# Optimization experiments

Hardware: AMD Instinct MI355X
Metric: run time of the kernel (lower is better)

Reference implementation:

```python
import math
import jax, jax.numpy as jnp
import numpy as np
from jax.scipy.special import ndtri

D = 128          # head_dim
BITS = 4         # bits per coordinate
NLEV = 1 << BITS # 16 codebook levels


def pack_indices(idx, bits):
    # idx: (..., d) uint8 with values < 2**bits; bits=4 -> 2 indices per byte.
    per_byte = 8 // bits
    i = idx.reshape(*idx.shape[:-1], idx.shape[-1] // per_byte, per_byte).astype(jnp.uint8)
    shifts = (jnp.arange(per_byte, dtype=jnp.uint8) * bits)  # low nibble first
    packed = jnp.zeros(i.shape[:-1], dtype=jnp.uint8)
    for j in range(per_byte):
        packed = packed | (i[..., j] << shifts[j])
    return packed


def unpack_indices(packed, bits, d):
    per_byte = 8 // bits
    mask = jnp.uint8((1 << bits) - 1)
    parts = [((packed >> jnp.uint8(j * bits)) & mask) for j in range(per_byte)]
    idx = jnp.stack(parts, axis=-1)  # (..., d_packed, per_byte)
    return idx.reshape(*packed.shape[:-1], d)


def setup_inputs() -> dict:
    key = jax.random.key(0)
    kx, kp = jax.random.split(key)
    x = jax.random.normal(kx, (4, 8, 4096, D), dtype=jnp.float32)
    # Random rotation matrix via QR of a Gaussian (orthogonal, like get_rotation_matrix).
    A = jax.random.normal(kp, (D, D), dtype=jnp.float32)
    Pi, _ = jnp.linalg.qr(A)
    # Lloyd-Max-style Gaussian codebook: sorted inverse-CDF midpoints of N(0,1).
    codebook = ndtri((jnp.arange(NLEV, dtype=jnp.float32) + 0.5) / NLEV).astype(jnp.float32)
    return {"x": x, "Pi": Pi.astype(jnp.float32), "codebook": codebook}


def reference(x, Pi, codebook):
    d = x.shape[-1]
    sqrt_d = math.sqrt(d)
    # ---- compress ----
    norms = jnp.linalg.norm(x, axis=-1)                       # (*batch,)
    x_unit = x / jnp.clip(norms, 1e-8)[..., None]
    x_rot_scaled = (x_unit @ Pi.T) * sqrt_d                   # (*batch, d)
    dists = jnp.abs(x_rot_scaled[..., None] - codebook)      # (*batch, d, n_levels)
    indices = jnp.argmin(dists, axis=-1).astype(jnp.uint8)   # (*batch, d)
    packed = pack_indices(indices, BITS)                      # (*batch, d_packed) uint8
    norms16 = norms.astype(jnp.float16)
    # ---- decompress ----
    idx = unpack_indices(packed, BITS, d).astype(jnp.int32)
    x_rot_hat = codebook[idx] / sqrt_d                        # (*batch, d)
    x_unit_hat = x_rot_hat @ Pi
    x_hat = x_unit_hat * norms16.astype(jnp.float32)[..., None]
    return x_hat
```

## Files before the change

### kernel.cpp

```cpp
#include <hip/hip_runtime.h>
#include <hip/hip_fp16.h>
#include <cstdint>

#define D 128
#define NLEV 16
#define TPB 512
#define WPB 8
#define RPW 8
#define NBATCH 2
#define ROWS_PER_WAVE 16
#define ROWS_PER_BLOCK (WPB * ROWS_PER_WAVE)

typedef __attribute__((ext_vector_type(8))) short bf16x8;
typedef __attribute__((ext_vector_type(4))) float f32x4;

__device__ __forceinline__ float rlane_f(float v, int l) {
    return __int_as_float(__builtin_amdgcn_readlane(__float_as_int(v), l));
}
__device__ __forceinline__ float sload_f(float v) {
    return __int_as_float(__builtin_amdgcn_readfirstlane(__float_as_int(v)));
}
__device__ __forceinline__ unsigned short f32_bf16(float f) {
    uint32_t u = __float_as_uint(f);
    return (unsigned short)((u + 0x7fffu + ((u >> 16) & 1u)) >> 16);
}
__device__ __forceinline__ float bf16_f32(unsigned short h) {
    return __uint_as_float(((uint32_t)h) << 16);
}

__global__ void tq_prepack(const float* __restrict__ Pi, float* __restrict__ PiT,
                           unsigned short* __restrict__ Bhi, unsigned short* __restrict__ Blo) {
    const int t = blockIdx.x * blockDim.x + threadIdx.x;
    PiT[t] = Pi[(t & (D - 1)) * D + (t >> 7)];
    const int e = t & 7, l = (t >> 3) & 63, f = t >> 9;
    const int kf = f & 3, it = f >> 2;
    const int k = kf * 32 + (l >> 4) * 8 + e;
    const int i = it * 16 + (l & 15);
    const float v = Pi[k * D + i];
    const unsigned short hi = f32_bf16(v);
    Bhi[t] = hi;
    Blo[t] = f32_bf16(v - bf16_f32(hi));
}

__global__ __launch_bounds__(TPB, 3)
void tq_main(const float* __restrict__ x, const float* __restrict__ PiT,
             const unsigned short* __restrict__ Bhi, const unsigned short* __restrict__ Blo,
             const float* __restrict__ cbk, float* __restrict__ out, int nrows) {
    __shared__ uint32_t lds_u[8192];
    float* ldsP = (float*)lds_u;

    const int tid  = threadIdx.x;
    const int lane = tid & 63;
    const int wave = tid >> 6;

    float code[NLEV], mid[NLEV - 1];
#pragma unroll
    for (int k = 0; k < NLEV; ++k) code[k] = sload_f(cbk[k]);
#pragma unroll
    for (int k = 0; k < NLEV - 1; ++k) mid[k] = 0.5f * (code[k] + code[k + 1]);

    const float sqrt_d = 11.313708498984761f;

    const int row0 = (blockIdx.x * WPB + wave) * ROWS_PER_WAVE;

    float2 xv[NBATCH][RPW];
#pragma unroll
    for (int b = 0; b < NBATCH; ++b)
#pragma unroll
        for (int r = 0; r < RPW; ++r) {
            int row = row0 + b * RPW + r;
            if (row >= nrows) row = nrows - 1;
            xv[b][r] = *reinterpret_cast<const float2*>(x + (size_t)row * D + 2 * lane);
        }

    float ns[NBATCH][RPW];
#pragma unroll
    for (int b = 0; b < NBATCH; ++b)
#pragma unroll
        for (int r = 0; r < RPW; ++r) {
            float s = fmaf(xv[b][r].x, xv[b][r].x, xv[b][r].y * xv[b][r].y);
#pragma unroll
            for (int off = 32; off; off >>= 1) s += __shfl_xor(s, off, 64);
            ns[b][r] = s;
        }

    float y0[NBATCH][RPW], y1[NBATCH][RPW];
#pragma unroll
    for (int b = 0; b < NBATCH; ++b)
#pragma unroll
        for (int r = 0; r < RPW; ++r) { y0[b][r] = 0.f; y1[b][r] = 0.f; }

    for (int h = 0; h < 2; ++h) {
        __syncthreads();
        for (int kk = tid; kk < 64 * D; kk += TPB) ldsP[kk] = PiT[h * 64 * D + kk];
        __syncthreads();
#pragma unroll 4
        for (int jj = 0; jj < 64; jj += 2) {
            const float2 p0 = *reinterpret_cast<const float2*>(ldsP + jj * D + 2 * lane);
            const float2 p1 = *reinterpret_cast<const float2*>(ldsP + (jj + 1) * D + 2 * lane);
            const int sl = (h * 64 + jj) >> 1;
#pragma unroll
            for (int b = 0; b < NBATCH; ++b)
#pragma unroll
                for (int r = 0; r < RPW; ++r) {
                    const float xa = rlane_f(xv[b][r].x, sl);
                    const float xb = rlane_f(xv[b][r].y, sl);
                    y0[b][r] = fmaf(p0.x, xa, y0[b][r]);
                    y1[b][r] = fmaf(p0.y, xa, y1[b][r]);
                    y0[b][r] = fmaf(p1.x, xb, y0[b][r]);
                    y1[b][r] = fmaf(p1.y, xb, y1[b][r]);
                }
        }
    }

    uint32_t cpk[NBATCH][RPW];
#pragma unroll
    for (int b = 0; b < NBATCH; ++b)
#pragma unroll
        for (int r = 0; r < RPW; ++r) {
            const float nrm = sqrtf(ns[b][r]);
            const float s1  = sqrt_d / fmaxf(nrm, 1e-8f);
            const float hh  = __half2float(__float2half(nrm));
            const float sc  = hh / sqrt_d;
            const float ya = y0[b][r] * s1;
            const float yb = y1[b][r] * s1;
            float ca = code[0], cb2 = code[0];
#pragma unroll
            for (int k = 0; k < NLEV - 1; ++k) {
                ca  = (ya > mid[k]) ? code[k + 1] : ca;
                cb2 = (yb > mid[k]) ? code[k + 1] : cb2;
            }
            const unsigned short ha = __half_as_ushort(__float2half(ca * sc));
            const unsigned short hb = __half_as_ushort(__float2half(cb2 * sc));
            cpk[b][r] = (uint32_t)ha | ((uint32_t)hb << 16);
        }

    __syncthreads();

#pragma unroll
    for (int b = 0; b < NBATCH; ++b)
#pragma unroll
        for (int r = 0; r < RPW; ++r) {
            const int r16 = b * RPW + r;
            lds_u[(wave * 16 + r16) * 64 + (lane ^ ((r16 & 7) << 2))] = cpk[b][r];
        }
    __syncthreads();

    const int m  = lane & 15;
    const int kb = lane >> 4;
    bf16x8 ahi[4], alo[4];
#pragma unroll
    for (int kf = 0; kf < 4; ++kf) {
        const int idx = (wave * 16 + m) * 64 + ((kf * 16 + kb * 4) ^ ((m & 7) << 2));
        const uint4 u = *reinterpret_cast<const uint4*>(lds_u + idx);
#pragma unroll
        for (int q = 0; q < 4; ++q) {
            const uint32_t w = ((const uint32_t*)&u)[q];
            const float f0 = __half2float(__ushort_as_half((unsigned short)(w & 0xffffu)));
            const float f1 = __half2float(__ushort_as_half((unsigned short)(w >> 16)));
            const unsigned short h0 = f32_bf16(f0);
            const unsigned short h1 = f32_bf16(f1);
            ahi[kf][2 * q]     = (short)h0;
            ahi[kf][2 * q + 1] = (short)h1;
            alo[kf][2 * q]     = (short)f32_bf16(f0 - bf16_f32(h0));
            alo[kf][2 * q + 1] = (short)f32_bf16(f1 - bf16_f32(h1));
        }
    }
#pragma unroll
    for (int it = 0; it < 8; ++it) {
        f32x4 a = {0.f, 0.f, 0.f, 0.f};
#pragma unroll
        for (int kf = 0; kf < 4; ++kf) {
            const size_t fi = (size_t)((it * 4 + kf) * 64 + lane) * 8;
            const bf16x8 bh = *reinterpret_cast<const bf16x8*>(Bhi + fi);
            const bf16x8 bl = *reinterpret_cast<const bf16x8*>(Blo + fi);
            a = __builtin_amdgcn_mfma_f32_16x16x32_bf16(ahi[kf], bh, a, 0, 0, 0);
            a = __builtin_amdgcn_mfma_f32_16x16x32_bf16(alo[kf], bh, a, 0, 0, 0);
            a = __builtin_amdgcn_mfma_f32_16x16x32_bf16(ahi[kf], bl, a, 0, 0, 0);
        }
#pragma unroll
        for (int reg = 0; reg < 4; ++reg) {
            const int row = row0 + kb * 4 + reg;
            if (row < nrows) out[(size_t)row * D + it * 16 + m] = a[reg];
        }
    }
}

extern "C" void kernel_launch(void* const* d_in, const int* in_sizes, int n_in,
                              void* d_out, int out_size, void* d_ws, size_t ws_size,
                              hipStream_t stream) {
    const float* x   = (const float*)d_in[0];
    const float* Pi  = (const float*)d_in[1];
    const float* cbk = (const float*)d_in[2];
    float* out = (float*)d_out;

    float*          PiT = (float*)d_ws;
    unsigned short* Bhi = (unsigned short*)((char*)d_ws + 65536);
    unsigned short* Blo = (unsigned short*)((char*)d_ws + 98304);

    const int nrows = in_sizes[0] / D;
    const int grid  = (nrows + ROWS_PER_BLOCK - 1) / ROWS_PER_BLOCK;

    tq_prepack<<<dim3(64), dim3(256), 0, stream>>>(Pi, PiT, Bhi, Blo);
    tq_main<<<dim3(grid), dim3(TPB), 0, stream>>>(x, PiT, Bhi, Blo, cbk, out, nrows);
}
```

Baseline: 234.7 us.

## Replace readlane broadcasts with uniform global loads and pair-packed Pi layout

The rotation GEMV no longer broadcasts x elements with per-row readlane. Each wave instead reads the x values it needs as wave-uniform float2 loads from global memory (cached). Pi is repacked so one float4 LDS load supplies two columns by two k-values, which halves the LDS load count. Rows are clamped to full 16-row tiles, and launch bounds drop from 3 to 2 blocks per CU, allowing more registers at the cost of occupancy.

```diff
diff --git a/kernel.cpp b/kernel.cpp
--- a/kernel.cpp
+++ b/kernel.cpp
@@ -6,17 +6,12 @@
 #define NLEV 16
 #define TPB 512
 #define WPB 8
-#define RPW 8
-#define NBATCH 2
 #define ROWS_PER_WAVE 16
 #define ROWS_PER_BLOCK (WPB * ROWS_PER_WAVE)
 
 typedef __attribute__((ext_vector_type(8))) short bf16x8;
 typedef __attribute__((ext_vector_type(4))) float f32x4;
 
-__device__ __forceinline__ float rlane_f(float v, int l) {
-    return __int_as_float(__builtin_amdgcn_readlane(__float_as_int(v), l));
-}
 __device__ __forceinline__ float sload_f(float v) {
     return __int_as_float(__builtin_amdgcn_readfirstlane(__float_as_int(v)));
 }
@@ -28,10 +23,13 @@
     return __uint_as_float(((uint32_t)h) << 16);
 }
 
-__global__ void tq_prepack(const float* __restrict__ Pi, float* __restrict__ PiT,
+__global__ void tq_prepack(const float* __restrict__ Pi, float* __restrict__ PiTpair,
                            unsigned short* __restrict__ Bhi, unsigned short* __restrict__ Blo) {
     const int t = blockIdx.x * blockDim.x + threadIdx.x;
-    PiT[t] = Pi[(t & (D - 1)) * D + (t >> 7)];
+    {
+        const int q = t & 3, l = (t >> 2) & 63, jp = t >> 8;
+        PiTpair[t] = Pi[(2 * l + (q & 1)) * D + (2 * jp + (q >> 1))];
+    }
     const int e = t & 7, l = (t >> 3) & 63, f = t >> 9;
     const int kf = f & 3, it = f >> 2;
     const int k = kf * 32 + (l >> 4) * 8 + e;
@@ -42,8 +40,8 @@
     Blo[t] = f32_bf16(v - bf16_f32(hi));
 }
 
-__global__ __launch_bounds__(TPB, 3)
-void tq_main(const float* __restrict__ x, const float* __restrict__ PiT,
+__global__ __launch_bounds__(TPB, 2)
+void tq_main(const float* __restrict__ x, const float* __restrict__ PiTpair,
              const unsigned short* __restrict__ Bhi, const unsigned short* __restrict__ Blo,
              const float* __restrict__ cbk, float* __restrict__ out, int nrows) {
     __shared__ uint32_t lds_u[8192];
@@ -61,89 +59,80 @@
 
     const float sqrt_d = 11.313708498984761f;
 
-    const int row0 = (blockIdx.x * WPB + wave) * ROWS_PER_WAVE;
+    int row0 = (blockIdx.x * WPB + wave) * ROWS_PER_WAVE;
+    if (row0 > nrows - ROWS_PER_WAVE) row0 = nrows - ROWS_PER_WAVE;
 
-    float2 xv[NBATCH][RPW];
+    float ns[ROWS_PER_WAVE];
+    {
+        float2 xv[ROWS_PER_WAVE];
 #pragma unroll
-    for (int b = 0; b < NBATCH; ++b)
+        for (int r = 0; r < ROWS_PER_WAVE; ++r)
+            xv[r] = *reinterpret_cast<const float2*>(x + (size_t)(row0 + r) * D + 2 * lane);
 #pragma unroll
-        for (int r = 0; r < RPW; ++r) {
-            int row = row0 + b * RPW + r;
-            if (row >= nrows) row = nrows - 1;
-            xv[b][r] = *reinterpret_cast<const float2*>(x + (size_t)row * D + 2 * lane);
-        }
-
-    float ns[NBATCH][RPW];
-#pragma unroll
-    for (int b = 0; b < NBATCH; ++b)
-#pragma unroll
-        for (int r = 0; r < RPW; ++r) {
-            float s = fmaf(xv[b][r].x, xv[b][r].x, xv[b][r].y * xv[b][r].y);
+        for (int r = 0; r < ROWS_PER_WAVE; ++r) {
+            float s = fmaf(xv[r].x, xv[r].x, xv[r].y * xv[r].y);
 #pragma unroll
             for (int off = 32; off; off >>= 1) s += __shfl_xor(s, off, 64);
-            ns[b][r] = s;
+            ns[r] = s;
         }
+    }
 
-    float y0[NBATCH][RPW], y1[NBATCH][RPW];
+    float y0[ROWS_PER_WAVE], y1[ROWS_PER_WAVE];
 #pragma unroll
-    for (int b = 0; b < NBATCH; ++b)
-#pragma unroll
-        for (int r = 0; r < RPW; ++r) { y0[b][r] = 0.f; y1[b][r] = 0.f; }
+    for (int r = 0; r < ROWS_PER_WAVE; ++r) { y0[r] = 0.f; y1[r] = 0.f; }
+
+    const float* xw = x + (size_t)row0 * D;
 
     for (int h = 0; h < 2; ++h) {
         __syncthreads();
-        for (int kk = tid; kk < 64 * D; kk += TPB) ldsP[kk] = PiT[h * 64 * D + kk];
+        {
+            const float4* src = reinterpret_cast<const float4*>(PiTpair + h * 8192);
+            float4* dst = reinterpret_cast<float4*>(ldsP);
+#pragma unroll
+            for (int k = 0; k < 4; ++k) dst[tid + k * TPB] = src[tid + k * TPB];
+        }
         __syncthreads();
-#pragma unroll 4
-        for (int jj = 0; jj < 64; jj += 2) {
-            const float2 p0 = *reinterpret_cast<const float2*>(ldsP + jj * D + 2 * lane);
-            const float2 p1 = *reinterpret_cast<const float2*>(ldsP + (jj + 1) * D + 2 * lane);
-            const int sl = (h * 64 + jj) >> 1;
+#pragma unroll 2
+        for (int jp = 0; jp < 32; ++jp) {
+            const float4 p = reinterpret_cast<const float4*>(ldsP)[jp * 64 + lane];
+            const int j = h * 64 + jp * 2;
 #pragma unroll
-            for (int b = 0; b < NBATCH; ++b)
-#pragma unroll
-                for (int r = 0; r < RPW; ++r) {
-                    const float xa = rlane_f(xv[b][r].x, sl);
-                    const float xb = rlane_f(xv[b][r].y, sl);
-                    y0[b][r] = fmaf(p0.x, xa, y0[b][r]);
-                    y1[b][r] = fmaf(p0.y, xa, y1[b][r]);
-                    y0[b][r] = fmaf(p1.x, xb, y0[b][r]);
-                    y1[b][r] = fmaf(p1.y, xb, y1[b][r]);
-                }
+            for (int r = 0; r < ROWS_PER_WAVE; ++r) {
+                const float2 xj = *reinterpret_cast<const float2*>(xw + r * D + j);
+                y0[r] = fmaf(p.x, xj.x, y0[r]);
+                y1[r] = fmaf(p.y, xj.x, y1[r]);
+                y0[r] = fmaf(p.z, xj.y, y0[r]);
+                y1[r] = fmaf(p.w, xj.y, y1[r]);
+            }
         }
     }
 
-    uint32_t cpk[NBATCH][RPW];
+    uint32_t cpk[ROWS_PER_WAVE];
 #pragma unroll
-    for (int b = 0; b < NBATCH; ++b)
+    for (int r = 0; r < ROWS_PER_WAVE; ++r) {
+        const float nrm = sqrtf(ns[r]);
+        const float s1  = sqrt_d / fmaxf(nrm, 1e-8f);
+        const float hh  = __half2float(__float2half(nrm));
+        const float sc  = hh / sqrt_d;
+        const float ya = y0[r] * s1;
+        const float yb = y1[r] * s1;
+        float ca = code[0], cb2 = code[0];
 #pragma unroll
-        for (int r = 0; r < RPW; ++r) {
-            const float nrm = sqrtf(ns[b][r]);
-            const float s1  = sqrt_d / fmaxf(nrm, 1e-8f);
-            const float hh  = __half2float(__float2half(nrm));
-            const float sc  = hh / sqrt_d;
-            const float ya = y0[b][r] * s1;
-            const float yb = y1[b][r] * s1;
-            float ca = code[0], cb2 = code[0];
-#pragma unroll
-            for (int k = 0; k < NLEV - 1; ++k) {
-                ca  = (ya > mid[k]) ? code[k + 1] : ca;
-                cb2 = (yb > mid[k]) ? code[k + 1] : cb2;
-            }
-            const unsigned short ha = __half_as_ushort(__float2half(ca * sc));
-            const unsigned short hb = __half_as_ushort(__float2half(cb2 * sc));
-            cpk[b][r] = (uint32_t)ha | ((uint32_t)hb << 16);
+        for (int k = 0; k < NLEV - 1; ++k) {
+            ca  = (ya > mid[k]) ? code[k + 1] : ca;
+            cb2 = (yb > mid[k]) ? code[k + 1] : cb2;
         }
+        const unsigned short ha = __half_as_ushort(__float2half(ca * sc));
+        const unsigned short hb = __half_as_ushort(__float2half(cb2 * sc));
+        cpk[r] = (uint32_t)ha | ((uint32_t)hb << 16);
+    }
 
     __syncthreads();
 
 #pragma unroll
-    for (int b = 0; b < NBATCH; ++b)
-#pragma unroll
-        for (int r = 0; r < RPW; ++r) {
-            const int r16 = b * RPW + r;
-            lds_u[(wave * 16 + r16) * 64 + (lane ^ ((r16 & 7) << 2))] = cpk[b][r];
-        }
+    for (int r = 0; r < ROWS_PER_WAVE; ++r) {
+        lds_u[(wave * 16 + r) * 64 + (lane ^ ((r & 7) << 2))] = cpk[r];
+    }
     __syncthreads();
 
     const int m  = lane & 15;
@@ -194,13 +183,13 @@
     const float* cbk = (const float*)d_in[2];
     float* out = (float*)d_out;
 
-    float*          PiT = (float*)d_ws;
+    float*          PiTpair = (float*)d_ws;
     unsigned short* Bhi = (unsigned short*)((char*)d_ws + 65536);
     unsigned short* Blo = (unsigned short*)((char*)d_ws + 98304);
 
     const int nrows = in_sizes[0] / D;
     const int grid  = (nrows + ROWS_PER_BLOCK - 1) / ROWS_PER_BLOCK;
 
-    tq_prepack<<<dim3(64), dim3(256), 0, stream>>>(Pi, PiT, Bhi, Blo);
-    tq_main<<<dim3(grid), dim3(TPB), 0, stream>>>(x, PiT, Bhi, Blo, cbk, out, nrows);
+    tq_prepack<<<dim3(64), dim3(256), 0, stream>>>(Pi, PiTpair, Bhi, Blo);
+    tq_main<<<dim3(grid), dim3(TPB), 0, stream>>>(x, PiTpair, Bhi, Blo, cbk, out, nrows);
 }
```

Result: slower. 287.0 us (+22.3%).
